# Kernel optimization log

Hardware: AMD Instinct MI355X
Metric: run time of the kernel (lower is better)

Reference implementation:

```python
import jax, jax.numpy as jnp
import numpy as np

BINS = 10          # init kwarg `bins`
LOSS_WEIGHT = 1.0  # init kwarg `loss_weight`


def setup_inputs() -> dict:
    key = jax.random.key(0)
    k1, k2, k3 = jax.random.split(key, 3)
    B, C = 131072, 80  # [batch_num(anchors), class_num]
    pred = jax.random.normal(k1, (B, C), dtype=jnp.float32)
    target = jax.random.randint(k2, (B, C), 0, 2).astype(jnp.int32)
    label_weight = jax.random.randint(k3, (B, C), 0, 2).astype(jnp.int32)
    return {"pred": pred, "target": target, "label_weight": label_weight}


def _ghmc_loss(pred, target_f, valid_f):
    # total number of valid samples (>=1), matches max(valid.sum().item(), 1.0)
    total = jnp.maximum(valid_f.sum(), 1.0)

    # gradient magnitude g = |sigmoid(pred).detach() - target|, in [0, 1]
    g = jnp.abs(jax.nn.sigmoid(jax.lax.stop_gradient(pred)) - target_f)

    # bin index: edges are i/bins, last edge padded by 1e-6, so
    # floor(g * bins) clipped to [0, bins-1] reproduces the torch loop's
    # per-element assignment (elements exactly on an edge take the later bin,
    # matching the sequential overwrite of weights[inds]).
    bin_idx = jnp.clip(jnp.floor(g * BINS).astype(jnp.int32), 0, BINS - 1)

    # histogram of valid elements per bin (invalid routed to extra bin BINS)
    flat_idx = jnp.where(valid_f > 0, bin_idx, BINS).reshape(-1)
    counts = jnp.bincount(flat_idx, length=BINS + 1)[:BINS].astype(pred.dtype)

    # n = number of non-empty bins (>=1 whenever any element is valid)
    n = jnp.maximum((counts > 0).sum(), 1).astype(pred.dtype)

    # per-bin weight total/num_in_bin, zero for empty bins, then /n
    w_bin = jnp.where(counts > 0, total / jnp.maximum(counts, 1.0), 0.0) / n
    weights = jnp.where(valid_f > 0, w_bin[bin_idx], 0.0)
    weights = jax.lax.stop_gradient(weights)  # histogram weights are detached

    # weighted BCE-with-logits, reduction='sum', then / total
    bce = target_f * jax.nn.softplus(-pred) + (1.0 - target_f) * jax.nn.softplus(pred)
    return (weights * bce).sum() / total * LOSS_WEIGHT


def reference(pred, target, label_weight):
    target_f = target.astype(pred.dtype)
    valid_f = (label_weight > 0).astype(pred.dtype)
    return _ghmc_loss(pred, target_f, valid_f)
```

## Files before the change

### kernel.cpp

```cpp
#include <hip/hip_runtime.h>

#define BINS 10
#define TPB  256
#define NB_MAX 2048
#define FTPB 1024
#define KPACK 4096.0f

__global__ __launch_bounds__(TPB, 4) void ghmc_hist_kernel(
    const float4* __restrict__ pred4,
    const int4*   __restrict__ tgt4,
    const int4*   __restrict__ lw4,
    float* __restrict__ part,
    int n4, int n)
{
    float acc[BINS];
#pragma unroll
    for (int b = 0; b < BINS; ++b) acc[b] = 0.f;

    auto proc = [&](float p, int t, int w) {
        float q     = __int_as_float(__float_as_int(p) ^ (t << 31));
        float e     = __expf(-fabsf(q));
        float d     = 1.f + e;
        float r     = __builtin_amdgcn_rcpf(d);
        float num   = (q >= 0.f) ? 1.0f : e;
        float sig10 = num * (10.f * r);
        int bin     = (int)sig10;
        bin = bin < (BINS - 1) ? bin : (BINS - 1);
        float bce   = fmaxf(q, 0.f) + __logf(d);
        float v     = (w > 0) ? (bce + KPACK) : 0.f;
        int bit     = 1 << bin;
        int vbits   = __float_as_int(v);
#pragma unroll
        for (int b = 0; b < BINS; ++b) {
            int sel = __builtin_amdgcn_sbfe(bit, b, 1);
            acc[b] += __int_as_float(sel & vbits);
        }
    };

    const int tid    = threadIdx.x;
    const int stride = gridDim.x * TPB;
    const int base   = blockIdx.x * TPB + tid;

    if (n4 == 5 * stride && (n & 3) == 0) {
        float4 P[5]; int4 T[5]; int4 W[5];
#pragma unroll
        for (int k = 0; k < 5; ++k) P[k] = pred4[base + k * stride];
#pragma unroll
        for (int k = 0; k < 5; ++k) T[k] = tgt4[base + k * stride];
#pragma unroll
        for (int k = 0; k < 5; ++k) W[k] = lw4[base + k * stride];
#pragma unroll
        for (int k = 0; k < 5; ++k) {
            proc(P[k].x, T[k].x, W[k].x);
            proc(P[k].y, T[k].y, W[k].y);
            proc(P[k].z, T[k].z, W[k].z);
            proc(P[k].w, T[k].w, W[k].w);
        }
    } else {
        const int full = n4 / stride;
        int i = base;
        float4 pA; int4 tA, wA;
        if (full > 0) { pA = pred4[i]; tA = tgt4[i]; wA = lw4[i]; }
        for (int k = 0; k < full - 1; ++k) {
            const int j = i + stride;
            float4 pB = pred4[j]; int4 tB = tgt4[j]; int4 wB = lw4[j];
            proc(pA.x, tA.x, wA.x); proc(pA.y, tA.y, wA.y);
            proc(pA.z, tA.z, wA.z); proc(pA.w, tA.w, wA.w);
            pA = pB; tA = tB; wA = wB;
            i = j;
        }
        if (full > 0) {
            proc(pA.x, tA.x, wA.x); proc(pA.y, tA.y, wA.y);
            proc(pA.z, tA.z, wA.z); proc(pA.w, tA.w, wA.w);
        }
        const int j = base + full * stride;
        if (j < n4) {
            float4 p = pred4[j]; int4 t = tgt4[j]; int4 w = lw4[j];
            proc(p.x, t.x, w.x); proc(p.y, t.y, w.y);
            proc(p.z, t.z, w.z); proc(p.w, t.w, w.w);
        }
        if (blockIdx.x == 0 && tid < (n & 3)) {
            const float* predf = (const float*)pred4;
            const int*   tgtf  = (const int*)tgt4;
            const int*   lwf   = (const int*)lw4;
            const int jj = n4 * 4 + tid;
            proc(predf[jj], tgtf[jj], lwf[jj]);
        }
    }

    float s_[BINS], c_[BINS];
#pragma unroll
    for (int b = 0; b < BINS; ++b) {
        float Cf = floorf(acc[b] * (1.f / KPACK));
        c_[b] = Cf;
        s_[b] = acc[b] - KPACK * Cf;
    }

#pragma unroll
    for (int b = 0; b < BINS; ++b) {
#pragma unroll
        for (int off = 1; off <= 8; off <<= 1) {
            s_[b] += __shfl_xor(s_[b], off, 64);
            c_[b] += __shfl_xor(c_[b], off, 64);
        }
    }

    __shared__ float red[2 * BINS][16];
    const int grp = tid >> 4;
    if ((tid & 15) == 0) {
#pragma unroll
        for (int b = 0; b < BINS; ++b) {
            red[b][grp]        = s_[b];
            red[BINS + b][grp] = c_[b];
        }
    }
    __syncthreads();
    if (tid < 2 * BINS) {
        float v = 0.f;
#pragma unroll
        for (int g = 0; g < 16; ++g) v += red[tid][g];
        part[blockIdx.x * (2 * BINS) + tid] = v;
    }
}

__global__ __launch_bounds__(FTPB) void ghmc_final_kernel(
    const float* __restrict__ part, float* __restrict__ out, int nb)
{
    float acc[2 * BINS];
#pragma unroll
    for (int v = 0; v < 2 * BINS; ++v) acc[v] = 0.f;

    const int tid = threadIdx.x;
    for (int i = tid; i < nb; i += FTPB) {
        const float4* rec = (const float4*)(part + (size_t)i * (2 * BINS));
        float4 a = rec[0], b = rec[1], c = rec[2], d = rec[3], e = rec[4];
        acc[0]  += a.x; acc[1]  += a.y; acc[2]  += a.z; acc[3]  += a.w;
        acc[4]  += b.x; acc[5]  += b.y; acc[6]  += b.z; acc[7]  += b.w;
        acc[8]  += c.x; acc[9]  += c.y; acc[10] += c.z; acc[11] += c.w;
        acc[12] += d.x; acc[13] += d.y; acc[14] += d.z; acc[15] += d.w;
        acc[16] += e.x; acc[17] += e.y; acc[18] += e.z; acc[19] += e.w;
    }

#pragma unroll
    for (int v = 0; v < 2 * BINS; ++v) {
#pragma unroll
        for (int off = 1; off <= 32; off <<= 1)
            acc[v] += __shfl_xor(acc[v], off, 64);
    }

    __shared__ float sh[2 * BINS][16];
    const int wv = tid >> 6, lane = tid & 63;
    if (lane == 0) {
#pragma unroll
        for (int v = 0; v < 2 * BINS; ++v) sh[v][wv] = acc[v];
    }
    __syncthreads();
    if (tid < 2 * BINS) {
        float s = 0.f;
#pragma unroll
        for (int g = 0; g < 16; ++g) s += sh[tid][g];
        sh[tid][0] = s;
    }
    __syncthreads();

    if (tid == 0) {
        float ti = 0.f; int nbn = 0;
        float cnts[BINS];
#pragma unroll
        for (int b = 0; b < BINS; ++b) {
            cnts[b] = sh[BINS + b][0];
            ti += cnts[b];
            nbn += (cnts[b] > 0.f) ? 1 : 0;
        }
        float total = fmaxf(ti, 1.f);
        float nf    = (float)(nbn > 0 ? nbn : 1);
        float loss  = 0.f;
#pragma unroll
        for (int b = 0; b < BINS; ++b) {
            if (cnts[b] > 0.f) {
                float w = (total / cnts[b]) / nf;
                loss += w * sh[b][0];
            }
        }
        out[0] = loss / total * 1.0f;
    }
}

extern "C" void kernel_launch(void* const* d_in, const int* in_sizes, int n_in,
                              void* d_out, int out_size, void* d_ws, size_t ws_size,
                              hipStream_t stream)
{
    const float4* pred4 = (const float4*)d_in[0];
    const int4*   tgt4  = (const int4*)d_in[1];
    const int4*   lw4   = (const int4*)d_in[2];

    const int n  = in_sizes[0];
    const int n4 = n / 4;

    int nb = (n4 + TPB - 1) / TPB;
    if (nb > NB_MAX) nb = NB_MAX;
    int ws_cap = (int)(ws_size / (2 * BINS * sizeof(float)));
    if (nb > ws_cap) nb = ws_cap;
    if (nb < 1) nb = 1;

    float* part = (float*)d_ws;

    ghmc_hist_kernel<<<nb, TPB, 0, stream>>>(pred4, tgt4, lw4, part, n4, n);
    ghmc_final_kernel<<<1, FTPB, 0, stream>>>(part, (float*)d_out, nb);
}
```

Measured before the change: 41.04 us.

## Replace register bin accumulators with per-thread shared-memory histogram and LDS atomics

Each element's packed value now goes through an LDS atomicAdd into a per-thread shared histogram column, replacing the ten masked register adds per element. The block reduction also changes: shuffles are dropped and every thread does LDS atomics on a small shared table. The specialised fully unrolled batched-load path is removed, so only the generic loop remains. This trades ALU work for LDS atomic traffic, and the final table reduction puts all 256 threads contending on the same 20 addresses.

Measured after the change: 128.8 us. 3.14x slower.

```diff
diff --git a/kernel.cpp b/kernel.cpp
--- a/kernel.cpp
+++ b/kernel.cpp
@@ -13,9 +13,13 @@
     float* __restrict__ part,
     int n4, int n)
 {
-    float acc[BINS];
+    __shared__ float hist[BINS][TPB];
+    __shared__ float tbl[2 * BINS];
+
+    const int tid = threadIdx.x;
 #pragma unroll
-    for (int b = 0; b < BINS; ++b) acc[b] = 0.f;
+    for (int b = 0; b < BINS; ++b) hist[b][tid] = 0.f;
+    if (tid < 2 * BINS) tbl[tid] = 0.f;
 
     auto proc = [&](float p, int t, int w) {
         float q     = __int_as_float(__float_as_int(p) ^ (t << 31));
@@ -28,99 +32,64 @@
         bin = bin < (BINS - 1) ? bin : (BINS - 1);
         float bce   = fmaxf(q, 0.f) + __logf(d);
         float v     = (w > 0) ? (bce + KPACK) : 0.f;
-        int bit     = 1 << bin;
-        int vbits   = __float_as_int(v);
-#pragma unroll
-        for (int b = 0; b < BINS; ++b) {
-            int sel = __builtin_amdgcn_sbfe(bit, b, 1);
-            acc[b] += __int_as_float(sel & vbits);
-        }
+        atomicAdd(&hist[bin][tid], v);
     };
 
-    const int tid    = threadIdx.x;
+    const int tid_   = tid;
     const int stride = gridDim.x * TPB;
-    const int base   = blockIdx.x * TPB + tid;
+    const int base   = blockIdx.x * TPB + tid_;
+    const int full   = n4 / stride;
 
-    if (n4 == 5 * stride && (n & 3) == 0) {
-        float4 P[5]; int4 T[5]; int4 W[5];
-#pragma unroll
-        for (int k = 0; k < 5; ++k) P[k] = pred4[base + k * stride];
-#pragma unroll
-        for (int k = 0; k < 5; ++k) T[k] = tgt4[base + k * stride];
-#pragma unroll
-        for (int k = 0; k < 5; ++k) W[k] = lw4[base + k * stride];
-#pragma unroll
-        for (int k = 0; k < 5; ++k) {
-            proc(P[k].x, T[k].x, W[k].x);
-            proc(P[k].y, T[k].y, W[k].y);
-            proc(P[k].z, T[k].z, W[k].z);
-            proc(P[k].w, T[k].w, W[k].w);
-        }
-    } else {
-        const int full = n4 / stride;
-        int i = base;
-        float4 pA; int4 tA, wA;
-        if (full > 0) { pA = pred4[i]; tA = tgt4[i]; wA = lw4[i]; }
-        for (int k = 0; k < full - 1; ++k) {
-            const int j = i + stride;
-            float4 pB = pred4[j]; int4 tB = tgt4[j]; int4 wB = lw4[j];
-            proc(pA.x, tA.x, wA.x); proc(pA.y, tA.y, wA.y);
-            proc(pA.z, tA.z, wA.z); proc(pA.w, tA.w, wA.w);
-            pA = pB; tA = tB; wA = wB;
-            i = j;
-        }
-        if (full > 0) {
-            proc(pA.x, tA.x, wA.x); proc(pA.y, tA.y, wA.y);
-            proc(pA.z, tA.z, wA.z); proc(pA.w, tA.w, wA.w);
-        }
+    int i = base;
+    float4 pA; int4 tA, wA;
+    if (full > 0) { pA = pred4[i]; tA = tgt4[i]; wA = lw4[i]; }
+    for (int k = 0; k < full - 1; ++k) {
+        const int j = i + stride;
+        float4 pB = pred4[j]; int4 tB = tgt4[j]; int4 wB = lw4[j];
+        proc(pA.x, tA.x, wA.x); proc(pA.y, tA.y, wA.y);
+        proc(pA.z, tA.z, wA.z); proc(pA.w, tA.w, wA.w);
+        pA = pB; tA = tB; wA = wB;
+        i = j;
+    }
+    if (full > 0) {
+        proc(pA.x, tA.x, wA.x); proc(pA.y, tA.y, wA.y);
+        proc(pA.z, tA.z, wA.z); proc(pA.w, tA.w, wA.w);
+    }
+    {
         const int j = base + full * stride;
         if (j < n4) {
             float4 p = pred4[j]; int4 t = tgt4[j]; int4 w = lw4[j];
             proc(p.x, t.x, w.x); proc(p.y, t.y, w.y);
             proc(p.z, t.z, w.z); proc(p.w, t.w, w.w);
         }
-        if (blockIdx.x == 0 && tid < (n & 3)) {
-            const float* predf = (const float*)pred4;
-            const int*   tgtf  = (const int*)tgt4;
-            const int*   lwf   = (const int*)lw4;
-            const int jj = n4 * 4 + tid;
-            proc(predf[jj], tgtf[jj], lwf[jj]);
-        }
+    }
+    if (blockIdx.x == 0 && tid_ < (n & 3)) {
+        const float* predf = (const float*)pred4;
+        const int*   tgtf  = (const int*)tgt4;
+        const int*   lwf   = (const int*)lw4;
+        const int j = n4 * 4 + tid_;
+        proc(predf[j], tgtf[j], lwf[j]);
     }
 
-    float s_[BINS], c_[BINS];
-#pragma unroll
-    for (int b = 0; b < BINS; ++b) {
-        float Cf = floorf(acc[b] * (1.f / KPACK));
-        c_[b] = Cf;
-        s_[b] = acc[b] - KPACK * Cf;
-    }
+    __syncthreads();
 
-#pragma unroll
-    for (int b = 0; b < BINS; ++b) {
-#pragma unroll
-        for (int off = 1; off <= 8; off <<= 1) {
-            s_[b] += __shfl_xor(s_[b], off, 64);
-            c_[b] += __shfl_xor(c_[b], off, 64);
-        }
-    }
-
-    __shared__ float red[2 * BINS][16];
-    const int grp = tid >> 4;
-    if ((tid & 15) == 0) {
+    {
+        float s_sum = 0.f, s_cnt_dummy;
+        (void)s_cnt_dummy;
 #pragma unroll
         for (int b = 0; b < BINS; ++b) {
-            red[b][grp]        = s_[b];
-            red[BINS + b][grp] = c_[b];
+            float x  = hist[b][tid_];
+            float Cf = floorf(x * (1.f / KPACK));
+            float Sf = x - KPACK * Cf;
+            atomicAdd(&tbl[b], Sf);
+            atomicAdd(&tbl[BINS + b], Cf);
         }
+        (void)s_sum;
     }
     __syncthreads();
-    if (tid < 2 * BINS) {
-        float v = 0.f;
-#pragma unroll
-        for (int g = 0; g < 16; ++g) v += red[tid][g];
-        part[blockIdx.x * (2 * BINS) + tid] = v;
-    }
+
+    if (tid_ < 2 * BINS)
+        part[blockIdx.x * (2 * BINS) + tid_] = tbl[tid_];
 }
 
 __global__ __launch_bounds__(FTPB) void ghmc_final_kernel(
```
